# Kernel tuning notes

Hardware: AMD Instinct MI355X
Metric: run time of the kernel (lower is better)

## Reference

```python
import jax, jax.numpy as jnp
import numpy as np

NEG_SLOPE = 0.2

def _gat_layer(x, src, dst, W, a_src, a_dst, bias, concat):
    # x: [N, F_in]; W: [F_in, H*C]; a_src/a_dst: [H, C]; bias: [H*C] or [C]
    N = x.shape[0]
    H, C = a_src.shape
    h = (x @ W).reshape(N, H, C)                      # node features per head
    e_src = jnp.einsum('nhc,hc->nh', h, a_src)        # [N, H]
    e_dst = jnp.einsum('nhc,hc->nh', h, a_dst)        # [N, H]
    e = jax.nn.leaky_relu(e_src[src] + e_dst[dst], NEG_SLOPE)  # [E, H]
    # segment softmax over incoming edges of each destination node
    m = jax.ops.segment_max(e, dst, num_segments=N)   # [N, H]
    p = jnp.exp(e - m[dst])
    denom = jax.ops.segment_sum(p, dst, num_segments=N)
    alpha = p / denom[dst]                            # [E, H]
    msg = h[src] * alpha[:, :, None]                  # [E, H, C]
    out = jax.ops.segment_sum(msg, dst, num_segments=N)  # [N, H, C]
    if concat:
        out = out.reshape(N, H * C) + bias
    else:
        out = out.mean(axis=1) + bias
    return out, alpha


def setup_inputs() -> dict:
    key = jax.random.key(0)
    ks = jax.random.split(key, 12)
    N, E = 20000, 320000
    F_in, Ch, Co, H = 256, 64, 64, 8
    x = jax.random.normal(ks[0], (N, F_in), dtype=jnp.float32)
    edge_index = jax.random.randint(ks[1], (2, E), 0, N, dtype=jnp.int64)
    s = 0.05
    return {
        'x': x,
        'edge_index': edge_index,
        'W1': jax.random.normal(ks[2], (F_in, H * Ch), dtype=jnp.float32) * s,
        'att_src1': jax.random.normal(ks[3], (H, Ch), dtype=jnp.float32) * s,
        'att_dst1': jax.random.normal(ks[4], (H, Ch), dtype=jnp.float32) * s,
        'b1': jnp.zeros((H * Ch,), dtype=jnp.float32),
        'W2': jax.random.normal(ks[5], (H * Ch, H * Co), dtype=jnp.float32) * s,
        'att_src2': jax.random.normal(ks[6], (H, Co), dtype=jnp.float32) * s,
        'att_dst2': jax.random.normal(ks[7], (H, Co), dtype=jnp.float32) * s,
        'b2': jnp.zeros((Co,), dtype=jnp.float32),
    }


def reference(x, edge_index, W1, att_src1, att_dst1, b1, W2, att_src2, att_dst2, b2):
    N = x.shape[0]
    # PyG GATConv adds self-loops by default
    loop = jnp.arange(N, dtype=edge_index.dtype)
    src = jnp.concatenate([edge_index[0], loop])
    dst = jnp.concatenate([edge_index[1], loop])
    h1, alpha1 = _gat_layer(x, src, dst, W1, att_src1, att_dst1, b1, concat=True)
    h1 = jax.nn.relu(h1)
    h2, alpha2 = _gat_layer(h1, src, dst, W2, att_src2, att_dst2, b2, concat=False)
    return h2, alpha1, alpha2
```

## Files before the change

### kernel.cpp

```cpp
#include <hip/hip_runtime.h>

#define H 8
#define C 64
#define HC 512
#define NEG 0.2f

typedef __attribute__((ext_vector_type(8))) _Float16 half8v;
typedef __attribute__((ext_vector_type(4))) _Float16 half4v;
typedef __attribute__((ext_vector_type(4))) float f32x4;

__device__ __forceinline__ float leaky(float x) { return x > 0.f ? x : NEG * x; }

#define GLOAD_LDS16(gp, lp) \
  __builtin_amdgcn_global_load_lds((const __attribute__((address_space(1))) unsigned int*)(gp), \
                                   (__attribute__((address_space(3))) unsigned int*)(lp), 16, 0, 0)

__global__ void k_degree(const int* __restrict__ ei, int E, int N, int* __restrict__ deg) {
    int e = blockIdx.x * blockDim.x + threadIdx.x;
    int Et = E + N;
    if (e >= Et) return;
    int d = (e < E) ? ei[E + e] : (e - E);
    atomicAdd(&deg[d], 1);
}

__global__ __launch_bounds__(1024) void k_scan(const int* __restrict__ deg, int N, int* __restrict__ row_start) {
    __shared__ int part[1024];
    int t = threadIdx.x;
    int chunk = (N + 1023) >> 10;
    int lo = t * chunk, hi = min(lo + chunk, N);
    int s = 0;
    for (int i = lo; i < hi; ++i) s += deg[i];
    part[t] = s;
    __syncthreads();
    for (int off = 1; off < 1024; off <<= 1) {
        int v = (t >= off) ? part[t - off] : 0;
        __syncthreads();
        part[t] += v;
        __syncthreads();
    }
    int base = (t == 0) ? 0 : part[t - 1];
    for (int i = lo; i < hi; ++i) { row_start[i] = base; base += deg[i]; }
    if (t == 1023) row_start[N] = part[1023];
}

__global__ void k_fill(const int* __restrict__ ei, int E, int N,
                       const int* __restrict__ row_start, int* __restrict__ cursor,
                       int* __restrict__ csr_src, int* __restrict__ csr_eid) {
    int e = blockIdx.x * blockDim.x + threadIdx.x;
    int Et = E + N;
    if (e >= Et) return;
    int d, s;
    if (e < E) { s = ei[e]; d = ei[E + e]; } else { s = e - E; d = s; }
    int pos = atomicAdd(&cursor[d], 1);
    int idx = row_start[d] + pos;
    csr_src[idx] = s;
    csr_eid[idx] = e;
}

__global__ void k_tofp16(const float* __restrict__ in, _Float16* __restrict__ out, int n4) {
    int i = blockIdx.x * blockDim.x + threadIdx.x;
    if (i >= n4) return;
    float4 v = reinterpret_cast<const float4*>(in)[i];
    half4v h;
    h[0] = (_Float16)v.x; h[1] = (_Float16)v.y;
    h[2] = (_Float16)v.z; h[3] = (_Float16)v.w;
    reinterpret_cast<half4v*>(out)[i] = h;
}

__global__ void k_tsplit(const float* __restrict__ W, _Float16* __restrict__ th,
                         _Float16* __restrict__ tl, int K, int Nc) {
    int idx = blockIdx.x * blockDim.x + threadIdx.x;
    if (idx >= K * Nc) return;
    int c = idx / K, k = idx - c * K;
    float v = W[(long)k * Nc + c];
    _Float16 hh = (_Float16)v;
    th[idx] = hh;
    tl[idx] = (_Float16)(v - (float)hh);
}

__global__ __launch_bounds__(256) void k_gemm_mfma(const _Float16* __restrict__ A,
                                                   const _Float16* __restrict__ Bh,
                                                   const _Float16* __restrict__ Bl,
                                                   _Float16* __restrict__ Cc, int M, int K, int Pb, int Mpad,
                                                   const float* __restrict__ a_src, const float* __restrict__ a_dst,
                                                   float* __restrict__ e_src, float* __restrict__ e_dst) {
    __shared__ _Float16 lA[8192], lBh[8192], lBl[8192];
    int bid = blockIdx.x;
    int panel = ((bid >> 5) << 3) + (bid & 7);
    int colb  = (bid >> 3) & 3;
    if (panel >= Pb) return;
    int tid = threadIdx.x;
    int w = tid >> 6, lane = tid & 63;
    int wr = w >> 1, wc = w & 1;
    int r0 = panel * 128, c0 = colb * 128;
    f32x4 acc[4][4] = {};
    int frag_off = ((lane >> 4) * 16 + (lane & 15)) * 8;

    int rb0 = tid >> 6, kc0 = (tid >> 4) & 3, r16_0 = tid & 15;
    int rb1 = (256 + tid) >> 6, kc1 = ((256 + tid) >> 4) & 3;
    long gaBase0 = (long)(r0 + rb0 * 16 + r16_0) * K + kc0 * 8;
    long gbBase0 = (long)(c0 + rb0 * 16 + r16_0) * K + kc0 * 8;
    long gaBase1 = (long)(r0 + rb1 * 16 + r16_0) * K + kc1 * 8;
    long gbBase1 = (long)(c0 + rb1 * 16 + r16_0) * K + kc1 * 8;
    int ldst0 = (w * 64) * 8;
    int ldst1 = (256 + w * 64) * 8;

#define STAGE(buf, k0)  do { \
        int off = (buf) * 4096; \
        GLOAD_LDS16(A  + gaBase0 + (k0), lA  + off + ldst0); \
        GLOAD_LDS16(Bh + gbBase0 + (k0), lBh + off + ldst0); \
        GLOAD_LDS16(Bl + gbBase0 + (k0), lBl + off + ldst0); \
        GLOAD_LDS16(A  + gaBase1 + (k0), lA  + off + ldst1); \
        GLOAD_LDS16(Bh + gbBase1 + (k0), lBh + off + ldst1); \
        GLOAD_LDS16(Bl + gbBase1 + (k0), lBl + off + ldst1); \
    } while (0)

    int nk = K >> 5;
    STAGE(0, 0);
    __syncthreads();
    int cur = 0;
    for (int t = 0; t < nk; ++t) {
        if (t + 1 < nk) STAGE(cur ^ 1, (t + 1) * 32);
        int off = cur * 4096;
        half8v fa[4], fbh[4], fbl[4];
        #pragma unroll
        for (int m = 0; m < 4; ++m) {
            int sa = off + (wr * 4 + m) * 512 + frag_off;
            fa[m] = *reinterpret_cast<half8v*>(&lA[sa]);
            int sb = off + (wc * 4 + m) * 512 + frag_off;
            fbh[m] = *reinterpret_cast<half8v*>(&lBh[sb]);
            fbl[m] = *reinterpret_cast<half8v*>(&lBl[sb]);
        }
        #pragma unroll
        for (int m = 0; m < 4; ++m)
            #pragma unroll
            for (int n = 0; n < 4; ++n) {
                acc[m][n] = __builtin_amdgcn_mfma_f32_16x16x32_f16(fa[m], fbh[n], acc[m][n], 0, 0, 0);
                acc[m][n] = __builtin_amdgcn_mfma_f32_16x16x32_f16(fa[m], fbl[n], acc[m][n], 0, 0, 0);
            }
        __syncthreads();
        cur ^= 1;
    }
#undef STAGE

    int head = colb * 2 + wc;
    long hbase = (long)head * Mpad * 64;
    #pragma unroll
    for (int m = 0; m < 4; ++m)
        #pragma unroll
        for (int j = 0; j < 4; ++j) {
            int gr = r0 + wr * 64 + m * 16 + (lane >> 4) * 4 + j;
            if (gr < M) {
                #pragma unroll
                for (int n = 0; n < 4; ++n)
                    Cc[hbase + (long)gr * 64 + n * 16 + (lane & 15)] = (_Float16)acc[m][n][j];
            }
        }
    float asv[4], adv[4];
    #pragma unroll
    for (int nn = 0; nn < 4; ++nn) {
        asv[nn] = a_src[head * 64 + nn * 16 + (lane & 15)];
        adv[nn] = a_dst[head * 64 + nn * 16 + (lane & 15)];
    }
    #pragma unroll
    for (int m = 0; m < 4; ++m)
        #pragma unroll
        for (int j = 0; j < 4; ++j) {
            int gr = r0 + wr * 64 + m * 16 + (lane >> 4) * 4 + j;
            float es = 0.f, ed = 0.f;
            #pragma unroll
            for (int nn = 0; nn < 4; ++nn) {
                es = fmaf(acc[m][nn][j], asv[nn], es);
                ed = fmaf(acc[m][nn][j], adv[nn], ed);
            }
            #pragma unroll
            for (int o = 1; o < 16; o <<= 1) {
                es += __shfl_xor(es, o);
                ed += __shfl_xor(ed, o);
            }
            if ((lane & 15) == 0 && gr < M) {
                e_src[gr * 8 + head] = es;
                e_dst[gr * 8 + head] = ed;
            }
        }
}

__global__ __launch_bounds__(512) void k_edge(const float* __restrict__ e_src,
                                              const float* __restrict__ e_dst,
                                              const int* __restrict__ row_start,
                                              const int* __restrict__ csr_src,
                                              const int* __restrict__ csr_eid,
                                              float* __restrict__ inv_buf,
                                              float* __restrict__ alpha,
                                              int N) {
    int wid = threadIdx.x >> 6, lane = threadIdx.x & 63;
    int g = lane >> 5;
    int eg = (lane >> 3) & 3;
    int h = lane & 7;
    int n = blockIdx.x * 16 + wid * 2 + g;
    bool valid = (n < N);
    int nc = valid ? n : (N - 1);
    int row = row_start[nc];
    int deg = row_start[nc + 1] - row;
    float ed = e_dst[nc * 8 + h];
    int it = (deg + 3) >> 2;
    int itmax = max(it, __shfl_xor(it, 32));
    float psum = 0.f;
    for (int c = 0; c < itmax; ++c) {
        int e0 = c * 4 + eg;
        int idx = row + min(e0, deg - 1);
        int s = csr_src[idx];
        float p = (e0 < deg) ? __expf(leaky(e_src[s * 8 + h] + ed)) : 0.f;
        psum += p;
    }
    psum += __shfl_xor(psum, 8);
    psum += __shfl_xor(psum, 16);
    float inv = 1.0f / psum;
    if (valid && eg == 0) inv_buf[n * 8 + h] = inv;
    for (int c = 0; c < itmax; ++c) {
        int e0 = c * 4 + eg;
        int idx = row + min(e0, deg - 1);
        int s = csr_src[idx];
        int eid = csr_eid[idx];
        float p = (e0 < deg) ? __expf(leaky(e_src[s * 8 + h] + ed)) : 0.f;
        if (valid && e0 < deg)
            alpha[(long)eid * 8 + h] = p * inv;
    }
}

__global__ __launch_bounds__(512) void k_gather(const half8v* __restrict__ hp8,
                                                const float* __restrict__ e_src,
                                                const float* __restrict__ e_dst,
                                                const int* __restrict__ row_start,
                                                const int* __restrict__ csr_src,
                                                const float* __restrict__ inv_buf,
                                                const float* __restrict__ bias,
                                                _Float16* __restrict__ h1,
                                                _Float16* __restrict__ accq,
                                                int N, int Mpad, int concat) {
    int wid = threadIdx.x >> 6, lane = threadIdx.x & 63;
    int bid = blockIdx.x;
    int h = bid & 7;
    int g = lane >> 5;
    int eg = (lane >> 3) & 3;
    int cg = lane & 7;
    int n = (bid >> 3) * 16 + wid * 2 + g;
    bool valid = (n < N);
    int nc = valid ? n : (N - 1);
    long hoff = (long)h * Mpad * 8;
    int row = row_start[nc];
    int deg = row_start[nc + 1] - row;
    float ed = e_dst[nc * 8 + h];
    int it = (deg + 3) >> 2;
    int itmax = max(it, __shfl_xor(it, 32));
    float acc[8] = {};
    for (int c = 0; c < itmax; ++c) {
        int e0 = c * 4 + eg;
        int idx = row + min(e0, deg - 1);
        int s = csr_src[idx];
        float es = e_src[s * 8 + h];
        float p = (e0 < deg) ? __expf(leaky(es + ed)) : 0.f;
        half8v hv = hp8[hoff + (long)s * 8 + cg];
        #pragma unroll
        for (int k = 0; k < 8; ++k)
            acc[k] = fmaf((float)hv[k], p, acc[k]);
    }
    #pragma unroll
    for (int o = 8; o <= 16; o <<= 1)
        #pragma unroll
        for (int k = 0; k < 8; ++k)
            acc[k] += __shfl_xor(acc[k], o);
    if (!valid) return;
    float inv = inv_buf[n * 8 + h];
    if (eg == 0) {
        if (concat) {
            half8v hh;
            #pragma unroll
            for (int k = 0; k < 8; ++k) {
                float v = fmaf(acc[k], inv, bias[h * 64 + cg * 8 + k]);
                v = v > 0.f ? v : 0.f;
                hh[k] = (_Float16)v;
            }
            reinterpret_cast<half8v*>(h1)[(long)n * 64 + h * 8 + cg] = hh;
        } else {
            half8v hv2;
            #pragma unroll
            for (int k = 0; k < 8; ++k) hv2[k] = (_Float16)(acc[k] * inv);
            reinterpret_cast<half8v*>(accq)[hoff + (long)n * 8 + cg] = hv2;
        }
    }
}

__global__ void k_mean(const _Float16* __restrict__ accq, const float* __restrict__ bias,
                       float* __restrict__ out, int N, int Mpad) {
    int i = blockIdx.x * blockDim.x + threadIdx.x;
    if (i >= N * 8) return;
    int n = i >> 3, cg = i & 7;
    float s[8] = {};
    #pragma unroll
    for (int h = 0; h < 8; ++h) {
        half8v v = reinterpret_cast<const half8v*>(accq)[(long)h * Mpad * 8 + (long)n * 8 + cg];
        #pragma unroll
        for (int k = 0; k < 8; ++k) s[k] += (float)v[k];
    }
    float4 r0, r1;
    r0.x = s[0] * 0.125f + bias[cg * 8 + 0];
    r0.y = s[1] * 0.125f + bias[cg * 8 + 1];
    r0.z = s[2] * 0.125f + bias[cg * 8 + 2];
    r0.w = s[3] * 0.125f + bias[cg * 8 + 3];
    r1.x = s[4] * 0.125f + bias[cg * 8 + 4];
    r1.y = s[5] * 0.125f + bias[cg * 8 + 5];
    r1.z = s[6] * 0.125f + bias[cg * 8 + 6];
    r1.w = s[7] * 0.125f + bias[cg * 8 + 7];
    float4* o4 = reinterpret_cast<float4*>(out + (long)n * 64 + cg * 8);
    o4[0] = r0;
    o4[1] = r1;
}

extern "C" void kernel_launch(void* const* d_in, const int* in_sizes, int n_in,
                              void* d_out, int out_size, void* d_ws, size_t ws_size,
                              hipStream_t stream) {
    const float* x   = (const float*)d_in[0];
    const int*   ei  = (const int*)d_in[1];
    const float* W1  = (const float*)d_in[2];
    const float* as1 = (const float*)d_in[3];
    const float* ad1 = (const float*)d_in[4];
    const float* b1  = (const float*)d_in[5];
    const float* W2  = (const float*)d_in[6];
    const float* as2 = (const float*)d_in[7];
    const float* ad2 = (const float*)d_in[8];
    const float* b2  = (const float*)d_in[9];

    int N  = in_sizes[0] / 256;
    int E  = in_sizes[1] / 2;
    int Et = E + N;
    int K1 = 256;
    int Mb   = (N + 127) / 128;
    int Mpad = Mb * 128;

    float* out    = (float*)d_out;
    float* h2_out = out;
    float* alpha1 = out + (size_t)N * 64;
    float* alpha2 = alpha1 + (size_t)Et * H;

    _Float16* hpre = (_Float16*)d_ws;
    _Float16* h1   = hpre + (size_t)Mpad * HC;
    _Float16* accq = h1 + (size_t)Mpad * HC;
    _Float16* xh   = accq + (size_t)Mpad * HC;
    _Float16* W1th = xh + (size_t)Mpad * K1;
    _Float16* W1tl = W1th + (size_t)HC * K1;
    _Float16* W2th = W1tl + (size_t)HC * K1;
    _Float16* W2tl = W2th + (size_t)HC * HC;
    float* eS     = (float*)(W2tl + (size_t)HC * HC);
    float* eD     = eS + (size_t)N * H;
    float* invb   = eD + (size_t)N * H;
    int*   deg    = (int*)(invb + (size_t)N * H);
    int*   cursor = deg + N;
    int*   row_st = cursor + N;
    int*   csr_src= row_st + N + 1;
    int*   csr_eid= csr_src + Et;

    hipMemsetAsync(deg, 0, (size_t)2 * N * sizeof(int), stream);
    int tb = 256;
    k_degree<<<(Et + tb - 1) / tb, tb, 0, stream>>>(ei, E, N, deg);
    k_scan<<<1, 1024, 0, stream>>>(deg, N, row_st);
    k_fill<<<(Et + tb - 1) / tb, tb, 0, stream>>>(ei, E, N, row_st, cursor, csr_src, csr_eid);

    int n4 = N * K1 / 4;
    k_tofp16<<<(n4 + tb - 1) / tb, tb, 0, stream>>>(x, xh, n4);
    k_tsplit<<<(K1 * HC + tb - 1) / tb, tb, 0, stream>>>(W1, W1th, W1tl, K1, HC);
    k_tsplit<<<(HC * HC + tb - 1) / tb, tb, 0, stream>>>(W2, W2th, W2tl, HC, HC);

    int Pb8 = ((Mb + 7) / 8) * 8;
    int ggemm = Pb8 * 4;
    int gedge = (N + 15) / 16;
    int ggath = ((N + 15) / 16) * 8;
    k_gemm_mfma<<<ggemm, 256, 0, stream>>>(xh, W1th, W1tl, hpre, N, K1, Mb, Mpad, as1, ad1, eS, eD);
    k_edge<<<gedge, 512, 0, stream>>>(eS, eD, row_st, csr_src, csr_eid, invb, alpha1, N);
    k_gather<<<ggath, 512, 0, stream>>>((const half8v*)hpre, eS, eD, row_st, csr_src, invb,
                                        b1, h1, nullptr, N, Mpad, 1);
    k_gemm_mfma<<<ggemm, 256, 0, stream>>>(h1, W2th, W2tl, hpre, N, HC, Mb, Mpad, as2, ad2, eS, eD);
    k_edge<<<gedge, 512, 0, stream>>>(eS, eD, row_st, csr_src, csr_eid, invb, alpha2, N);
    k_gather<<<ggath, 512, 0, stream>>>((const half8v*)hpre, eS, eD, row_st, csr_src, invb,
                                        b2, nullptr, accq, N, Mpad, 0);
    k_mean<<<(N * 8 + tb - 1) / tb, tb, 0, stream>>>(accq, b2, h2_out, N, Mpad);
}
```

Before: 321.2 us.

## Store normalized alpha in CSR order and reuse it in gather with prefetch

```diff
diff --git a/kernel.cpp b/kernel.cpp
--- a/kernel.cpp
+++ b/kernel.cpp
@@ -190,8 +190,8 @@
                                               const int* __restrict__ row_start,
                                               const int* __restrict__ csr_src,
                                               const int* __restrict__ csr_eid,
-                                              float* __restrict__ inv_buf,
                                               float* __restrict__ alpha,
+                                              float* __restrict__ alp_csr,
                                               int N) {
     int wid = threadIdx.x >> 6, lane = threadIdx.x & 63;
     int g = lane >> 5;
@@ -216,24 +216,24 @@
     psum += __shfl_xor(psum, 8);
     psum += __shfl_xor(psum, 16);
     float inv = 1.0f / psum;
-    if (valid && eg == 0) inv_buf[n * 8 + h] = inv;
     for (int c = 0; c < itmax; ++c) {
         int e0 = c * 4 + eg;
         int idx = row + min(e0, deg - 1);
         int s = csr_src[idx];
         int eid = csr_eid[idx];
         float p = (e0 < deg) ? __expf(leaky(e_src[s * 8 + h] + ed)) : 0.f;
-        if (valid && e0 < deg)
-            alpha[(long)eid * 8 + h] = p * inv;
+        if (valid && e0 < deg) {
+            float a = p * inv;
+            alpha[(long)eid * 8 + h] = a;
+            alp_csr[(long)idx * 8 + h] = a;
+        }
     }
 }
 
 __global__ __launch_bounds__(512) void k_gather(const half8v* __restrict__ hp8,
-                                                const float* __restrict__ e_src,
-                                                const float* __restrict__ e_dst,
                                                 const int* __restrict__ row_start,
                                                 const int* __restrict__ csr_src,
-                                                const float* __restrict__ inv_buf,
+                                                const float* __restrict__ alp_csr,
                                                 const float* __restrict__ bias,
                                                 _Float16* __restrict__ h1,
                                                 _Float16* __restrict__ accq,
@@ -250,20 +250,26 @@
     long hoff = (long)h * Mpad * 8;
     int row = row_start[nc];
     int deg = row_start[nc + 1] - row;
-    float ed = e_dst[nc * 8 + h];
     int it = (deg + 3) >> 2;
     int itmax = max(it, __shfl_xor(it, 32));
     float acc[8] = {};
+    int idx0 = row + min(eg, deg - 1);
+    int s_pf = csr_src[idx0];
+    float a_pf = alp_csr[(long)idx0 * 8 + h];
     for (int c = 0; c < itmax; ++c) {
+        int s_cur = s_pf;
+        float a_cur = a_pf;
         int e0 = c * 4 + eg;
-        int idx = row + min(e0, deg - 1);
-        int s = csr_src[idx];
-        float es = e_src[s * 8 + h];
-        float p = (e0 < deg) ? __expf(leaky(es + ed)) : 0.f;
-        half8v hv = hp8[hoff + (long)s * 8 + cg];
+        if (c + 1 < itmax) {
+            int idxn = row + min(e0 + 4, deg - 1);
+            s_pf = csr_src[idxn];
+            a_pf = alp_csr[(long)idxn * 8 + h];
+        }
+        float a = (e0 < deg) ? a_cur : 0.f;
+        half8v hv = hp8[hoff + (long)s_cur * 8 + cg];
         #pragma unroll
         for (int k = 0; k < 8; ++k)
-            acc[k] = fmaf((float)hv[k], p, acc[k]);
+            acc[k] = fmaf((float)hv[k], a, acc[k]);
     }
     #pragma unroll
     for (int o = 8; o <= 16; o <<= 1)
@@ -271,13 +277,12 @@
         for (int k = 0; k < 8; ++k)
             acc[k] += __shfl_xor(acc[k], o);
     if (!valid) return;
-    float inv = inv_buf[n * 8 + h];
     if (eg == 0) {
         if (concat) {
             half8v hh;
             #pragma unroll
             for (int k = 0; k < 8; ++k) {
-                float v = fmaf(acc[k], inv, bias[h * 64 + cg * 8 + k]);
+                float v = acc[k] + bias[h * 64 + cg * 8 + k];
                 v = v > 0.f ? v : 0.f;
                 hh[k] = (_Float16)v;
             }
@@ -285,7 +290,7 @@
         } else {
             half8v hv2;
             #pragma unroll
-            for (int k = 0; k < 8; ++k) hv2[k] = (_Float16)(acc[k] * inv);
+            for (int k = 0; k < 8; ++k) hv2[k] = (_Float16)acc[k];
             reinterpret_cast<half8v*>(accq)[hoff + (long)n * 8 + cg] = hv2;
         }
     }
@@ -353,8 +358,8 @@
     _Float16* W2tl = W2th + (size_t)HC * HC;
     float* eS     = (float*)(W2tl + (size_t)HC * HC);
     float* eD     = eS + (size_t)N * H;
-    float* invb   = eD + (size_t)N * H;
-    int*   deg    = (int*)(invb + (size_t)N * H);
+    float* alpcsr = eD + (size_t)N * H;
+    int*   deg    = (int*)(alpcsr + (size_t)Et * H);
     int*   cursor = deg + N;
     int*   row_st = cursor + N;
     int*   csr_src= row_st + N + 1;
@@ -376,12 +381,12 @@
     int gedge = (N + 15) / 16;
     int ggath = ((N + 15) / 16) * 8;
     k_gemm_mfma<<<ggemm, 256, 0, stream>>>(xh, W1th, W1tl, hpre, N, K1, Mb, Mpad, as1, ad1, eS, eD);
-    k_edge<<<gedge, 512, 0, stream>>>(eS, eD, row_st, csr_src, csr_eid, invb, alpha1, N);
-    k_gather<<<ggath, 512, 0, stream>>>((const half8v*)hpre, eS, eD, row_st, csr_src, invb,
+    k_edge<<<gedge, 512, 0, stream>>>(eS, eD, row_st, csr_src, csr_eid, alpha1, alpcsr, N);
+    k_gather<<<ggath, 512, 0, stream>>>((const half8v*)hpre, row_st, csr_src, alpcsr,
                                         b1, h1, nullptr, N, Mpad, 1);
     k_gemm_mfma<<<ggemm, 256, 0, stream>>>(h1, W2th, W2tl, hpre, N, HC, Mb, Mpad, as2, ad2, eS, eD);
-    k_edge<<<gedge, 512, 0, stream>>>(eS, eD, row_st, csr_src, csr_eid, invb, alpha2, N);
-    k_gather<<<ggath, 512, 0, stream>>>((const half8v*)hpre, eS, eD, row_st, csr_src, invb,
+    k_edge<<<gedge, 512, 0, stream>>>(eS, eD, row_st, csr_src, csr_eid, alpha2, alpcsr, N);
+    k_gather<<<ggath, 512, 0, stream>>>((const half8v*)hpre, row_st, csr_src, alpcsr,
                                         b2, nullptr, accq, N, Mpad, 0);
     k_mean<<<(N * 8 + tb - 1) / tb, tb, 0, stream>>>(accq, b2, h2_out, N, Mpad);
 }
```

Result: faster. 286.2 us (-10.9%).

## Materialize unnormalized edge weights in CSR order and restructure alpha/gather pipeline

Applied to the files above, without the earlier changes.

```diff
diff --git a/kernel.cpp b/kernel.cpp
--- a/kernel.cpp
+++ b/kernel.cpp
@@ -45,7 +45,8 @@
 
 __global__ void k_fill(const int* __restrict__ ei, int E, int N,
                        const int* __restrict__ row_start, int* __restrict__ cursor,
-                       int* __restrict__ csr_src, int* __restrict__ csr_eid) {
+                       int* __restrict__ csr_src, int* __restrict__ csr_eid,
+                       int* __restrict__ csr_dst) {
     int e = blockIdx.x * blockDim.x + threadIdx.x;
     int Et = E + N;
     if (e >= Et) return;
@@ -55,6 +56,7 @@
     int idx = row_start[d] + pos;
     csr_src[idx] = s;
     csr_eid[idx] = e;
+    csr_dst[idx] = d;
 }
 
 __global__ void k_tofp16(const float* __restrict__ in, _Float16* __restrict__ out, int n4) {
@@ -81,9 +83,7 @@
 __global__ __launch_bounds__(256) void k_gemm_mfma(const _Float16* __restrict__ A,
                                                    const _Float16* __restrict__ Bh,
                                                    const _Float16* __restrict__ Bl,
-                                                   _Float16* __restrict__ Cc, int M, int K, int Pb, int Mpad,
-                                                   const float* __restrict__ a_src, const float* __restrict__ a_dst,
-                                                   float* __restrict__ e_src, float* __restrict__ e_dst) {
+                                                   _Float16* __restrict__ Cc, int M, int K, int Pb, int Mpad) {
     __shared__ _Float16 lA[8192], lBh[8192], lBl[8192];
     int bid = blockIdx.x;
     int panel = ((bid >> 5) << 3) + (bid & 7);
@@ -156,42 +156,48 @@
                     Cc[hbase + (long)gr * 64 + n * 16 + (lane & 15)] = (_Float16)acc[m][n][j];
             }
         }
-    float asv[4], adv[4];
-    #pragma unroll
-    for (int nn = 0; nn < 4; ++nn) {
-        asv[nn] = a_src[head * 64 + nn * 16 + (lane & 15)];
-        adv[nn] = a_dst[head * 64 + nn * 16 + (lane & 15)];
-    }
-    #pragma unroll
-    for (int m = 0; m < 4; ++m)
-        #pragma unroll
-        for (int j = 0; j < 4; ++j) {
-            int gr = r0 + wr * 64 + m * 16 + (lane >> 4) * 4 + j;
-            float es = 0.f, ed = 0.f;
-            #pragma unroll
-            for (int nn = 0; nn < 4; ++nn) {
-                es = fmaf(acc[m][nn][j], asv[nn], es);
-                ed = fmaf(acc[m][nn][j], adv[nn], ed);
-            }
-            #pragma unroll
-            for (int o = 1; o < 16; o <<= 1) {
-                es += __shfl_xor(es, o);
-                ed += __shfl_xor(ed, o);
-            }
-            if ((lane & 15) == 0 && gr < M) {
-                e_src[gr * 8 + head] = es;
-                e_dst[gr * 8 + head] = ed;
-            }
-        }
+}
+
+__global__ __launch_bounds__(512) void k_edot(const half8v* __restrict__ hp8,
+                                              const float* __restrict__ a_src,
+                                              const float* __restrict__ a_dst,
+                                              float* __restrict__ e_src, float* __restrict__ e_dst,
+                                              int N, int Mpad) {
+    int h = threadIdx.x >> 6, lane = threadIdx.x & 63;
+    int n8 = lane >> 3, cg = lane & 7;
+    int n = blockIdx.x * 8 + n8;
+    bool valid = (n < N);
+    int nc = valid ? n : (N - 1);
+    float as[8], ad[8];
+    #pragma unroll
+    for (int k = 0; k < 8; ++k) {
+        as[k] = a_src[h * 64 + cg * 8 + k];
+        ad[k] = a_dst[h * 64 + cg * 8 + k];
+    }
+    half8v hv = hp8[(long)h * Mpad * 8 + (long)nc * 8 + cg];
+    float es = 0.f, ed = 0.f;
+    #pragma unroll
+    for (int k = 0; k < 8; ++k) {
+        es = fmaf((float)hv[k], as[k], es);
+        ed = fmaf((float)hv[k], ad[k], ed);
+    }
+    #pragma unroll
+    for (int o = 1; o <= 4; o <<= 1) {
+        es += __shfl_xor(es, o);
+        ed += __shfl_xor(ed, o);
+    }
+    if (valid && cg == 0) {
+        e_src[n * 8 + h] = es;
+        e_dst[n * 8 + h] = ed;
+    }
 }
 
 __global__ __launch_bounds__(512) void k_edge(const float* __restrict__ e_src,
                                               const float* __restrict__ e_dst,
                                               const int* __restrict__ row_start,
                                               const int* __restrict__ csr_src,
-                                              const int* __restrict__ csr_eid,
+                                              float* __restrict__ alp_csr,
                                               float* __restrict__ inv_buf,
-                                              float* __restrict__ alpha,
                                               int N) {
     int wid = threadIdx.x >> 6, lane = threadIdx.x & 63;
     int g = lane >> 5;
@@ -212,27 +218,36 @@
         int s = csr_src[idx];
         float p = (e0 < deg) ? __expf(leaky(e_src[s * 8 + h] + ed)) : 0.f;
         psum += p;
+        if (valid && e0 < deg)
+            alp_csr[(long)idx * 8 + h] = p;
     }
     psum += __shfl_xor(psum, 8);
     psum += __shfl_xor(psum, 16);
     float inv = 1.0f / psum;
     if (valid && eg == 0) inv_buf[n * 8 + h] = inv;
-    for (int c = 0; c < itmax; ++c) {
-        int e0 = c * 4 + eg;
-        int idx = row + min(e0, deg - 1);
-        int s = csr_src[idx];
-        int eid = csr_eid[idx];
-        float p = (e0 < deg) ? __expf(leaky(e_src[s * 8 + h] + ed)) : 0.f;
-        if (valid && e0 < deg)
-            alpha[(long)eid * 8 + h] = p * inv;
-    }
+}
+
+__global__ void k_alpha(const int* __restrict__ csr_dst, const int* __restrict__ csr_eid,
+                        const float* __restrict__ alp_csr, const float* __restrict__ inv_buf,
+                        float* __restrict__ alpha, int Et) {
+    int idx = blockIdx.x * blockDim.x + threadIdx.x;
+    if (idx >= Et) return;
+    int d = csr_dst[idx], eid = csr_eid[idx];
+    const float4* p4 = reinterpret_cast<const float4*>(alp_csr) + (long)idx * 2;
+    const float4* i4 = reinterpret_cast<const float4*>(inv_buf) + (long)d * 2;
+    float4 p0 = p4[0], p1 = p4[1], i0 = i4[0], i1 = i4[1];
+    float4 r0, r1;
+    r0.x = p0.x * i0.x; r0.y = p0.y * i0.y; r0.z = p0.z * i0.z; r0.w = p0.w * i0.w;
+    r1.x = p1.x * i1.x; r1.y = p1.y * i1.y; r1.z = p1.z * i1.z; r1.w = p1.w * i1.w;
+    float4* o4 = reinterpret_cast<float4*>(alpha) + (long)eid * 2;
+    o4[0] = r0;
+    o4[1] = r1;
 }
 
 __global__ __launch_bounds__(512) void k_gather(const half8v* __restrict__ hp8,
-                                                const float* __restrict__ e_src,
-                                                const float* __restrict__ e_dst,
                                                 const int* __restrict__ row_start,
                                                 const int* __restrict__ csr_src,
+                                                const float* __restrict__ alp_csr,
                                                 const float* __restrict__ inv_buf,
                                                 const float* __restrict__ bias,
                                                 _Float16* __restrict__ h1,
@@ -250,20 +265,36 @@
     long hoff = (long)h * Mpad * 8;
     int row = row_start[nc];
     int deg = row_start[nc + 1] - row;
-    float ed = e_dst[nc * 8 + h];
-    int it = (deg + 3) >> 2;
+    float inv = inv_buf[nc * 8 + h];
+    int it = (deg + 7) >> 3;
     int itmax = max(it, __shfl_xor(it, 32));
     float acc[8] = {};
+    int idxA = row + min(eg, deg - 1);
+    int idxB = row + min(4 + eg, deg - 1);
+    int   sA = csr_src[idxA];
+    float aA = alp_csr[(long)idxA * 8 + h];
+    int   sB = csr_src[idxB];
+    float aB = alp_csr[(long)idxB * 8 + h];
     for (int c = 0; c < itmax; ++c) {
-        int e0 = c * 4 + eg;
-        int idx = row + min(e0, deg - 1);
-        int s = csr_src[idx];
-        float es = e_src[s * 8 + h];
-        float p = (e0 < deg) ? __expf(leaky(es + ed)) : 0.f;
-        half8v hv = hp8[hoff + (long)s * 8 + cg];
-        #pragma unroll
-        for (int k = 0; k < 8; ++k)
-            acc[k] = fmaf((float)hv[k], p, acc[k]);
+        int e0 = c * 8 + eg, e1 = e0 + 4;
+        int sA_c = sA, sB_c = sB;
+        float aA_c = (e0 < deg) ? aA : 0.f;
+        float aB_c = (e1 < deg) ? aB : 0.f;
+        if (c + 1 < itmax) {
+            int nA = row + min(e0 + 8, deg - 1);
+            int nB = row + min(e1 + 8, deg - 1);
+            sA = csr_src[nA];
+            aA = alp_csr[(long)nA * 8 + h];
+            sB = csr_src[nB];
+            aB = alp_csr[(long)nB * 8 + h];
+        }
+        half8v hA = hp8[hoff + (long)sA_c * 8 + cg];
+        half8v hB = hp8[hoff + (long)sB_c * 8 + cg];
+        #pragma unroll
+        for (int k = 0; k < 8; ++k) {
+            acc[k] = fmaf((float)hA[k], aA_c, acc[k]);
+            acc[k] = fmaf((float)hB[k], aB_c, acc[k]);
+        }
     }
     #pragma unroll
     for (int o = 8; o <= 16; o <<= 1)
@@ -271,7 +302,6 @@
         for (int k = 0; k < 8; ++k)
             acc[k] += __shfl_xor(acc[k], o);
     if (!valid) return;
-    float inv = inv_buf[n * 8 + h];
     if (eg == 0) {
         if (concat) {
             half8v hh;
@@ -353,18 +383,20 @@
     _Float16* W2tl = W2th + (size_t)HC * HC;
     float* eS     = (float*)(W2tl + (size_t)HC * HC);
     float* eD     = eS + (size_t)N * H;
-    float* invb   = eD + (size_t)N * H;
+    float* alpcsr = eD + (size_t)N * H;
+    float* invb   = alpcsr + (size_t)Et * H;
     int*   deg    = (int*)(invb + (size_t)N * H);
     int*   cursor = deg + N;
     int*   row_st = cursor + N;
     int*   csr_src= row_st + N + 1;
     int*   csr_eid= csr_src + Et;
+    int*   csr_dst= csr_eid + Et;
 
     hipMemsetAsync(deg, 0, (size_t)2 * N * sizeof(int), stream);
     int tb = 256;
     k_degree<<<(Et + tb - 1) / tb, tb, 0, stream>>>(ei, E, N, deg);
     k_scan<<<1, 1024, 0, stream>>>(deg, N, row_st);
-    k_fill<<<(Et + tb - 1) / tb, tb, 0, stream>>>(ei, E, N, row_st, cursor, csr_src, csr_eid);
+    k_fill<<<(Et + tb - 1) / tb, tb, 0, stream>>>(ei, E, N, row_st, cursor, csr_src, csr_eid, csr_dst);
 
     int n4 = N * K1 / 4;
     k_tofp16<<<(n4 + tb - 1) / tb, tb, 0, stream>>>(x, xh, n4);
@@ -373,15 +405,20 @@
 
     int Pb8 = ((Mb + 7) / 8) * 8;
     int ggemm = Pb8 * 4;
+    int gedot = (N + 7) / 8;
     int gedge = (N + 15) / 16;
     int ggath = ((N + 15) / 16) * 8;
-    k_gemm_mfma<<<ggemm, 256, 0, stream>>>(xh, W1th, W1tl, hpre, N, K1, Mb, Mpad, as1, ad1, eS, eD);
-    k_edge<<<gedge, 512, 0, stream>>>(eS, eD, row_st, csr_src, csr_eid, invb, alpha1, N);
-    k_gather<<<ggath, 512, 0, stream>>>((const half8v*)hpre, eS, eD, row_st, csr_src, invb,
+    k_gemm_mfma<<<ggemm, 256, 0, stream>>>(xh, W1th, W1tl, hpre, N, K1, Mb, Mpad);
+    k_edot<<<gedot, 512, 0, stream>>>((const half8v*)hpre, as1, ad1, eS, eD, N, Mpad);
+    k_edge<<<gedge, 512, 0, stream>>>(eS, eD, row_st, csr_src, alpcsr, invb, N);
+    k_alpha<<<(Et + tb - 1) / tb, tb, 0, stream>>>(csr_dst, csr_eid, alpcsr, invb, alpha1, Et);
+    k_gather<<<ggath, 512, 0, stream>>>((const half8v*)hpre, row_st, csr_src, alpcsr, invb,
                                         b1, h1, nullptr, N, Mpad, 1);
-    k_gemm_mfma<<<ggemm, 256, 0, stream>>>(h1, W2th, W2tl, hpre, N, HC, Mb, Mpad, as2, ad2, eS, eD);
-    k_edge<<<gedge, 512, 0, stream>>>(eS, eD, row_st, csr_src, csr_eid, invb, alpha2, N);
-    k_gather<<<ggath, 512, 0, stream>>>((const half8v*)hpre, eS, eD, row_st, csr_src, invb,
+    k_gemm_mfma<<<ggemm, 256, 0, stream>>>(h1, W2th, W2tl, hpre, N, HC, Mb, Mpad);
+    k_edot<<<gedot, 512, 0, stream>>>((const half8v*)hpre, as2, ad2, eS, eD, N, Mpad);
+    k_edge<<<gedge, 512, 0, stream>>>(eS, eD, row_st, csr_src, alpcsr, invb, N);
+    k_alpha<<<(Et + tb - 1) / tb, tb, 0, stream>>>(csr_dst, csr_eid, alpcsr, invb, alpha2, Et);
+    k_gather<<<ggath, 512, 0, stream>>>((const half8v*)hpre, row_st, csr_src, alpcsr, invb,
                                         b2, nullptr, accq, N, Mpad, 0);
     k_mean<<<(N * 8 + tb - 1) / tb, tb, 0, stream>>>(accq, b2, h2_out, N, Mpad);
 }
```

After: 280.5 us. 12.7% less time.
